# Optimization experiments

Hardware: AMD Instinct MI355X
Metric: run time of the kernel (lower is better)

The kernel has to match this reference:

```python
import jax, jax.numpy as jnp
import numpy as np
import math

B, S, D_EMB = 1, 4096, 768
N_HEADS, D_QKV = 12, 64
INV_TEMP = 1.0


def setup_inputs() -> dict:
    key = jax.random.key(0)
    ks = jax.random.split(key, 11)
    s = 0.02
    return {
        "q_in": jax.random.normal(ks[0], (B, S, D_EMB), jnp.float32),
        "k_in": jax.random.normal(ks[1], (B, S, D_EMB), jnp.float32),
        "v_in": jax.random.normal(ks[2], (B, S, D_EMB), jnp.float32),
        "W_q": jax.random.normal(ks[3], (D_EMB, N_HEADS * D_QKV), jnp.float32) * s,
        "b_q": jnp.zeros((N_HEADS * D_QKV,), jnp.float32),
        "W_k": jax.random.normal(ks[4], (D_EMB, N_HEADS * D_QKV), jnp.float32) * s,
        "b_k": jnp.zeros((N_HEADS * D_QKV,), jnp.float32),
        "W_v": jax.random.normal(ks[5], (D_EMB, N_HEADS * D_QKV), jnp.float32) * s,
        "b_v": jnp.zeros((N_HEADS * D_QKV,), jnp.float32),
        "W_o": jax.random.normal(ks[6], (N_HEADS * D_QKV, D_EMB), jnp.float32) * s,
        "b_o": jnp.zeros((D_EMB,), jnp.float32),
    }


def _split_heads(x):  # [B,S,H*D] -> [B,H,S,D]
    b, s, _ = x.shape
    return x.reshape(b, s, N_HEADS, D_QKV).transpose(0, 2, 1, 3)


def reference(q_in, k_in, v_in, W_q, b_q, W_k, b_k, W_v, b_v, W_o, b_o):
    q = _split_heads(q_in @ W_q + b_q)
    k = _split_heads(k_in @ W_k + b_k)
    v = _split_heads(v_in @ W_v + b_v)
    # full [B,H,S,S] score matrix (module materializes it for custom masking)
    scores = INV_TEMP * jnp.einsum('bhqd,bhkd->bhqk', q, k) / math.sqrt(D_QKV)
    attn = jax.nn.softmax(scores, axis=-1)
    out = jnp.einsum('bhqk,bhkd->bhqd', attn, v)  # [B,H,S,D]
    out = out.transpose(0, 2, 1, 3).reshape(q_in.shape[0], q_in.shape[1], N_HEADS * D_QKV)
    return out @ W_o + b_o
```

## Files before the change

### kernel.cpp

```cpp
#include <hip/hip_runtime.h>

#define S 4096
#define E 768
#define NH 12
#define DH 64
#define QSCALE (0.125f * 1.44269504f)
#define KSPLIT 4

typedef __bf16 bf16;
typedef __bf16 bf16x4 __attribute__((ext_vector_type(4)));
typedef __bf16 bf16x8 __attribute__((ext_vector_type(8)));
typedef float  f32x4  __attribute__((ext_vector_type(4)));

#define MFMA(a, b, c) __builtin_amdgcn_mfma_f32_16x16x32_bf16(a, b, c, 0, 0, 0)

__device__ __forceinline__ void async16(const bf16* g, bf16* l) {
  __builtin_amdgcn_global_load_lds(
      (const __attribute__((address_space(1))) void*)g,
      (__attribute__((address_space(3))) void*)l, 16, 0, 0);
}

__global__ __launch_bounds__(256) void prologue(const float* __restrict__ q_in,
                                                const float* __restrict__ k_in,
                                                const float* __restrict__ v_in,
                                                const float* __restrict__ w0,
                                                const float* __restrict__ w1,
                                                const float* __restrict__ w2,
                                                const float* __restrict__ w3,
                                                bf16* __restrict__ qb,
                                                bf16* __restrict__ kb,
                                                bf16* __restrict__ vb,
                                                bf16* __restrict__ t0,
                                                bf16* __restrict__ t1,
                                                bf16* __restrict__ t2,
                                                bf16* __restrict__ t3) {
  const int bid = blockIdx.x, tid = threadIdx.x;
  if (bid < 2304) {
    const int z = bid / 576, rem = bid % 576;
    const int bx = rem % 24, by = rem / 24;
    const float* W = z == 0 ? w0 : (z == 1 ? w1 : (z == 2 ? w2 : w3));
    bf16* Wt = z == 0 ? t0 : (z == 1 ? t1 : (z == 2 ? t2 : t3));
    __shared__ float t[32][33];
    const int tx = tid & 31, ty = tid >> 5;
    for (int j = ty; j < 32; j += 8)
      t[j][tx] = W[(by * 32 + j) * E + bx * 32 + tx];
    __syncthreads();
    for (int j = ty; j < 32; j += 8)
      Wt[(bx * 32 + j) * E + by * 32 + tx] = (bf16)t[tx][j];
  } else {
    const int b2 = bid - 2304;
    const int z = b2 / 3072, r2 = b2 % 3072;
    const float* in = z == 0 ? q_in : (z == 1 ? k_in : v_in);
    bf16* out = z == 0 ? qb : (z == 1 ? kb : vb);
    const int i = r2 * 1024 + tid * 4;
    float4 v = *(const float4*)(in + i);
    bf16x4 o = { (bf16)v.x, (bf16)v.y, (bf16)v.z, (bf16)v.w };
    *(bf16x4*)(out + i) = o;
  }
}

__global__ __launch_bounds__(256) void gemm128(const bf16* __restrict__ A0,
                                               const bf16* __restrict__ A1,
                                               const bf16* __restrict__ A2,
                                               const bf16* __restrict__ B0,
                                               const bf16* __restrict__ B1,
                                               const bf16* __restrict__ B2,
                                               const float* __restrict__ bias0,
                                               const float* __restrict__ bias1,
                                               const float* __restrict__ bias2,
                                               bf16* __restrict__ C0,
                                               bf16* __restrict__ C1,
                                               bf16* __restrict__ C2) {
  __shared__ __align__(16) bf16 smem[128 * 136];
  bf16* Asm = smem;
  bf16* Bsm = smem + 4096;
  bf16* Cs  = smem;

  const int z = blockIdx.z;
  const bf16* A  = z == 0 ? A0 : (z == 1 ? A1 : A2);
  const bf16* Bt = z == 0 ? B0 : (z == 1 ? B1 : B2);
  const float* bias = z == 0 ? bias0 : (z == 1 ? bias1 : bias2);

  const int tid = threadIdx.x;
  const int wv = tid >> 6, lane = tid & 63;
  const int quad = lane >> 4, l16 = lane & 15;
  const int m0 = blockIdx.x * 128, n0 = blockIdx.y * 128;
  const int wm = (wv >> 1) * 64, wn = (wv & 1) * 64;
  const int srow = lane >> 2, scol = (lane & 3) * 8;

  f32x4 acc[4][4] = {};

  for (int k0 = 0; k0 < E; k0 += 32) {
#pragma unroll
    for (int j = 0; j < 2; j++) {
      const int ch = wv * 2 + j;
      async16(&A[(size_t)(m0 + ch * 16 + srow) * E + k0 + scol], &Asm[ch * 512]);
      async16(&Bt[(size_t)(n0 + ch * 16 + srow) * E + k0 + scol], &Bsm[ch * 512]);
    }
    __syncthreads();
    bf16x8 af[4], bfv[4];
#pragma unroll
    for (int mi = 0; mi < 4; mi++)
      af[mi] = *(const bf16x8*)&Asm[(wm + mi * 16 + l16) * 32 + quad * 8];
#pragma unroll
    for (int ni = 0; ni < 4; ni++)
      bfv[ni] = *(const bf16x8*)&Bsm[(wn + ni * 16 + l16) * 32 + quad * 8];
#pragma unroll
    for (int mi = 0; mi < 4; mi++)
#pragma unroll
      for (int ni = 0; ni < 4; ni++)
        acc[mi][ni] = MFMA(af[mi], bfv[ni], acc[mi][ni]);
    __syncthreads();
  }

  const float scale = (z == 0) ? QSCALE : 1.0f;
#pragma unroll
  for (int mi = 0; mi < 4; mi++) {
#pragma unroll
    for (int ni = 0; ni < 4; ni++) {
      const int nl = wn + ni * 16 + l16;
      const float bv = bias[n0 + nl];
#pragma unroll
      for (int r = 0; r < 4; r++) {
        const int ml = wm + mi * 16 + quad * 4 + r;
        const float v = (acc[mi][ni][r] + bv) * scale;
        if (z == 2) Cs[nl * 136 + ml] = (bf16)v;
        else        Cs[ml * 136 + nl] = (bf16)v;
      }
    }
  }
  __syncthreads();

  if (z == 0) {
    const int e = lane & 7;
#pragma unroll
    for (int p = 0; p < 8; p++) {
      const int hr = p * 32 + wv * 8 + (lane >> 3);
      const int r = hr >> 1, hf = hr & 1;
      bf16x8 c = *(const bf16x8*)&Cs[r * 136 + hf * 64 + e * 8];
      *(bf16x8*)(C0 + (size_t)((n0 >> 6) + hf) * S * DH + (size_t)(m0 + r) * DH + e * 8) = c;
    }
  } else {
    bf16* dst = (z == 1) ? C1 : C2;
#pragma unroll
    for (int p = 0; p < 8; p++) {
      const int cid = p * 4 + wv;
      const int reg = cid >> 3;
      const int i = cid & 7;
      const int h_l = reg >> 1, tile = reg & 1;
      bf16x8 c;
      if (z == 1) {
        const int row = tile * 64 + (i >> 1) * 16 + l16;
        const int col = h_l * 64 + (i & 1) * 32 + quad * 8;
        c = *(const bf16x8*)&Cs[row * 136 + col];
      } else {
        const int nl = h_l * 64 + (i >> 1) * 16 + l16;
        const int ml = tile * 64 + (i & 1) * 32 + quad * 8;
        c = *(const bf16x8*)&Cs[nl * 136 + ml];
      }
      *(bf16x8*)(dst + (size_t)((n0 >> 6) + h_l) * S * DH +
                 (size_t)((m0 >> 6) + tile) * 4096 + i * 512 + lane * 8) = c;
    }
  }
}

__global__ __launch_bounds__(256, 3) void attn(const bf16* __restrict__ Q,
                                               const bf16* __restrict__ Kf,
                                               const bf16* __restrict__ Vf,
                                               bf16* __restrict__ Op0,
                                               bf16* __restrict__ Op1,
                                               bf16* __restrict__ Op2,
                                               bf16* __restrict__ Op3,
                                               float* __restrict__ Lp) {
  __shared__ __align__(16) bf16 P2[4][64][72];
  const int h = blockIdx.y, ks = blockIdx.z;
  const int tid = threadIdx.x;
  const int wave = tid >> 6, lane = tid & 63;
  const int quad = lane >> 4, l16 = lane & 15;
  const int q0 = blockIdx.x * 256 + wave * 64;

  const bf16* Qh = Q + (size_t)h * S * DH;
  const bf16* kbase = Kf + (size_t)h * S * DH + (size_t)ks * (S / KSPLIT) * DH + lane * 8;
  const bf16* vbase = Vf + (size_t)h * S * DH + (size_t)ks * (S / KSPLIT) * DH + lane * 8;
  bf16* Op = ks == 0 ? Op0 : (ks == 1 ? Op1 : (ks == 2 ? Op2 : Op3));

  bf16x8 aq[4][2];
#pragma unroll
  for (int qb = 0; qb < 4; qb++)
#pragma unroll
    for (int j = 0; j < 2; j++)
      aq[qb][j] = *(const bf16x8*)&Qh[(size_t)(q0 + qb * 16 + l16) * DH + j * 32 + quad * 8];

  bf16x8 ones;
#pragma unroll
  for (int e = 0; e < 8; e++) ones[e] = (bf16)1.0f;

  f32x4 o[4][4] = {};
  f32x4 ol[4] = {};

  bf16* Pw = &P2[wave][0][0];

  const int T = (S / KSPLIT) / 64;
  for (int t = 0; t < T; ++t) {
    const bf16* kp = kbase + (size_t)t * 4096;
    bf16x8 kr[8];
#pragma unroll
    for (int i = 0; i < 8; i++) kr[i] = *(const bf16x8*)(kp + i * 512);

#pragma unroll
    for (int kb = 0; kb < 4; kb++)
#pragma unroll
      for (int qb = 0; qb < 4; qb++) {
        f32x4 st = {};
        st = MFMA(kr[kb * 2], aq[qb][0], st);
        st = MFMA(kr[kb * 2 + 1], aq[qb][1], st);
        bf16x4 pk;
#pragma unroll
        for (int r = 0; r < 4; r++) pk[r] = (bf16)__builtin_exp2f(st[r]);
        *(bf16x4*)&Pw[(qb * 16 + l16) * 72 + kb * 16 + quad * 4] = pk;
      }

    bf16x8 bp[4][2];
#pragma unroll
    for (int qb = 0; qb < 4; qb++)
#pragma unroll
      for (int jc = 0; jc < 2; jc++)
        bp[qb][jc] = *(const bf16x8*)&Pw[(qb * 16 + l16) * 72 + jc * 32 + quad * 8];

#pragma unroll
    for (int qb = 0; qb < 4; qb++) {
      ol[qb] = MFMA(ones, bp[qb][0], ol[qb]);
      ol[qb] = MFMA(ones, bp[qb][1], ol[qb]);
    }

    const bf16* vp = vbase + (size_t)t * 4096;
#pragma unroll
    for (int db = 0; db < 4; db++) {
      bf16x8 v0 = *(const bf16x8*)(vp + (db * 2) * 512);
      bf16x8 v1 = *(const bf16x8*)(vp + (db * 2 + 1) * 512);
#pragma unroll
      for (int qb = 0; qb < 4; qb++) {
        o[db][qb] = MFMA(v0, bp[qb][0], o[db][qb]);
        o[db][qb] = MFMA(v1, bp[qb][1], o[db][qb]);
      }
    }
  }

  float* Lph = Lp + (size_t)(ks * NH + h) * S;
  if (quad == 0) {
#pragma unroll
    for (int qb = 0; qb < 4; qb++)
      Lph[q0 + qb * 16 + l16] = ol[qb][0];
  }
#pragma unroll
  for (int db = 0; db < 4; db++)
#pragma unroll
    for (int qb = 0; qb < 4; qb++) {
      bf16x4 pk;
#pragma unroll
      for (int r = 0; r < 4; r++) pk[r] = (bf16)o[db][qb][r];
      *(bf16x4*)&Pw[(qb * 16 + l16) * 72 + db * 16 + quad * 4] = pk;
    }
  {
    const int rr = lane >> 3, ee = (lane & 7) * 8;
#pragma unroll
    for (int p = 0; p < 8; p++) {
      const int row = p * 8 + rr;
      bf16x8 c = *(const bf16x8*)&Pw[row * 72 + ee];
      *(bf16x8*)(Op + (size_t)(q0 + row) * E + h * DH + ee) = c;
    }
  }
}

__global__ __launch_bounds__(256) void combine(const bf16* __restrict__ Op0,
                                               const bf16* __restrict__ Op1,
                                               const bf16* __restrict__ Op2,
                                               const bf16* __restrict__ Op3,
                                               const float* __restrict__ Lp,
                                               bf16* __restrict__ Obf) {
  const int i8 = blockIdx.x * 256 + threadIdx.x;
  const size_t base = (size_t)i8 * 8;
  const int row = (int)(base / E), c = (int)(base % E);
  const int h = c >> 6;
  const float l = Lp[(size_t)h * S + row] + Lp[(size_t)(NH + h) * S + row] +
                  Lp[(size_t)(2 * NH + h) * S + row] + Lp[(size_t)(3 * NH + h) * S + row];
  const float rl = 1.0f / l;
  bf16x8 a = *(const bf16x8*)(Op0 + base);
  bf16x8 b = *(const bf16x8*)(Op1 + base);
  bf16x8 cc = *(const bf16x8*)(Op2 + base);
  bf16x8 d = *(const bf16x8*)(Op3 + base);
  bf16x8 o;
#pragma unroll
  for (int e = 0; e < 8; e++)
    o[e] = (bf16)((((float)a[e] + (float)b[e]) + ((float)cc[e] + (float)d[e])) * rl);
  *(bf16x8*)(Obf + base) = o;
}

__global__ __launch_bounds__(256) void gemm64(const bf16* __restrict__ A,
                                              const bf16* __restrict__ Bt,
                                              const float* __restrict__ bias,
                                              float* __restrict__ C) {
  __shared__ __align__(16) bf16 Asm[2][64 * 32];
  __shared__ __align__(16) bf16 Bsm[2][64 * 32];
  const int tid = threadIdx.x;
  const int wv = tid >> 6, lane = tid & 63;
  const int quad = lane >> 4, l16 = lane & 15;
  const int m0 = blockIdx.x * 64, n0 = blockIdx.y * 64;
  const int srow = lane >> 2, scol = (lane & 3) * 8;

  f32x4 acc[4] = {};

  for (int k0 = 0; k0 < E; k0 += 64) {
#pragma unroll
    for (int jc = 0; jc < 2; jc++) {
      async16(&A[(size_t)(m0 + wv * 16 + srow) * E + k0 + jc * 32 + scol], &Asm[jc][wv * 512]);
      async16(&Bt[(size_t)(n0 + wv * 16 + srow) * E + k0 + jc * 32 + scol], &Bsm[jc][wv * 512]);
    }
    __syncthreads();
#pragma unroll
    for (int jc = 0; jc < 2; jc++) {
      bf16x8 af = *(const bf16x8*)&Asm[jc][(wv * 16 + l16) * 32 + quad * 8];
#pragma unroll
      for (int ni = 0; ni < 4; ni++) {
        bf16x8 bfr = *(const bf16x8*)&Bsm[jc][(ni * 16 + l16) * 32 + quad * 8];
        acc[ni] = MFMA(af, bfr, acc[ni]);
      }
    }
    __syncthreads();
  }

  const int row0 = m0 + wv * 16 + quad * 4;
#pragma unroll
  for (int ni = 0; ni < 4; ni++) {
    const int col = n0 + ni * 16 + l16;
    const float bv = bias[col];
#pragma unroll
    for (int r = 0; r < 4; r++)
      C[(size_t)(row0 + r) * E + col] = acc[ni][r] + bv;
  }
}

extern "C" void kernel_launch(void* const* d_in, const int* in_sizes, int n_in,
                              void* d_out, int out_size, void* d_ws, size_t ws_size,
                              hipStream_t stream) {
  (void)in_sizes; (void)n_in; (void)out_size; (void)ws_size;
  const float* q_in = (const float*)d_in[0];
  const float* k_in = (const float*)d_in[1];
  const float* v_in = (const float*)d_in[2];
  const float* W_q  = (const float*)d_in[3];
  const float* b_q  = (const float*)d_in[4];
  const float* W_k  = (const float*)d_in[5];
  const float* b_k  = (const float*)d_in[6];
  const float* W_v  = (const float*)d_in[7];
  const float* b_v  = (const float*)d_in[8];
  const float* W_o  = (const float*)d_in[9];
  const float* b_o  = (const float*)d_in[10];

  const size_t SE2 = (size_t)S * E * 2;
  const size_t EE2 = (size_t)E * E * 2;
  char* ws = (char*)d_ws;
  bf16* qb  = (bf16*)(ws);
  bf16* kb  = (bf16*)(ws + SE2);
  bf16* vb  = (bf16*)(ws + 2 * SE2);
  bf16* WqT = (bf16*)(ws + 3 * SE2);
  bf16* WkT = (bf16*)(ws + 3 * SE2 + EE2);
  bf16* WvT = (bf16*)(ws + 3 * SE2 + 2 * EE2);
  bf16* WoT = (bf16*)(ws + 3 * SE2 + 3 * EE2);
  bf16* Qh  = (bf16*)(ws + 3 * SE2 + 4 * EE2);
  bf16* Kf  = (bf16*)(ws + 4 * SE2 + 4 * EE2);
  bf16* Vf  = (bf16*)(ws + 5 * SE2 + 4 * EE2);
  bf16* Obf = (bf16*)(ws + 6 * SE2 + 4 * EE2);
  bf16* Op1 = qb;
  bf16* Op2 = kb;
  bf16* Op3 = vb;
  float* Lp = (float*)WqT;

  prologue<<<dim3(2304 + 3 * 3072), 256, 0, stream>>>(
      q_in, k_in, v_in, W_q, W_k, W_v, W_o, qb, kb, vb, WqT, WkT, WvT, WoT);

  gemm128<<<dim3(S / 128, E / 128, 3), 256, 0, stream>>>(
      qb, kb, vb, WqT, WkT, WvT, b_q, b_k, b_v, Qh, Kf, Vf);

  attn<<<dim3(S / 256, NH, KSPLIT), 256, 0, stream>>>(Qh, Kf, Vf, Obf, Op1, Op2, Op3, Lp);

  combine<<<dim3(S * E / 2048), 256, 0, stream>>>(Obf, Op1, Op2, Op3, Lp, Obf);

  gemm64<<<dim3(S / 64, E / 64), 256, 0, stream>>>(Obf, WoT, b_o, (float*)d_out);
}
```

Before: 228.5 us.

## Double-buffer K/V tiles in LDS via async loads and swizzle block order

```diff
diff --git a/kernel.cpp b/kernel.cpp
--- a/kernel.cpp
+++ b/kernel.cpp
@@ -172,17 +172,37 @@
                                                bf16* __restrict__ Op2,
                                                bf16* __restrict__ Op3,
                                                float* __restrict__ Lp) {
-  __shared__ __align__(16) bf16 P2[4][64][72];
-  const int h = blockIdx.y, ks = blockIdx.z;
+  __shared__ __align__(16) bf16 Kbuf[2][4096];
+  __shared__ __align__(16) bf16 Vbuf[2][4096];
+  __shared__ __align__(16) bf16 P2[4][32][72];
+
+  const int flat = blockIdx.x + 16 * (blockIdx.y + 12 * blockIdx.z);
+  const int swz = (flat & 7) * 96 + (flat >> 3);
+  const int qt = swz & 15;
+  const int rem = swz >> 4;
+  const int ks = rem & 3;
+  const int h = rem >> 2;
+
   const int tid = threadIdx.x;
   const int wave = tid >> 6, lane = tid & 63;
   const int quad = lane >> 4, l16 = lane & 15;
-  const int q0 = blockIdx.x * 256 + wave * 64;
+  const int q0 = qt * 256 + wave * 64;
 
   const bf16* Qh = Q + (size_t)h * S * DH;
-  const bf16* kbase = Kf + (size_t)h * S * DH + (size_t)ks * (S / KSPLIT) * DH + lane * 8;
-  const bf16* vbase = Vf + (size_t)h * S * DH + (size_t)ks * (S / KSPLIT) * DH + lane * 8;
+  const bf16* kbase = Kf + (size_t)h * S * DH + (size_t)ks * (S / KSPLIT) * DH;
+  const bf16* vbase = Vf + (size_t)h * S * DH + (size_t)ks * (S / KSPLIT) * DH;
   bf16* Op = ks == 0 ? Op0 : (ks == 1 ? Op1 : (ks == 2 ? Op2 : Op3));
+
+  auto stageKV = [&](int buf, int t) {
+    const bf16* kg = kbase + (size_t)t * 4096 + wave * 1024 + lane * 8;
+    const bf16* vg = vbase + (size_t)t * 4096 + wave * 1024 + lane * 8;
+    async16(kg,       &Kbuf[buf][wave * 1024]);
+    async16(kg + 512, &Kbuf[buf][wave * 1024 + 512]);
+    async16(vg,       &Vbuf[buf][wave * 1024]);
+    async16(vg + 512, &Vbuf[buf][wave * 1024 + 512]);
+  };
+
+  stageKV(0, 0);
 
   bf16x8 aq[4][2];
 #pragma unroll
@@ -202,48 +222,62 @@
 
   const int T = (S / KSPLIT) / 64;
   for (int t = 0; t < T; ++t) {
-    const bf16* kp = kbase + (size_t)t * 4096;
+    if (t + 1 < T) {
+      stageKV((t + 1) & 1, t + 1);
+      asm volatile("s_waitcnt vmcnt(4)" ::: "memory");
+    } else {
+      asm volatile("s_waitcnt vmcnt(0)" ::: "memory");
+    }
+    asm volatile("s_barrier" ::: "memory");
+
+    const bf16* kp = &Kbuf[t & 1][lane * 8];
+    const bf16* vp = &Vbuf[t & 1][lane * 8];
     bf16x8 kr[8];
 #pragma unroll
     for (int i = 0; i < 8; i++) kr[i] = *(const bf16x8*)(kp + i * 512);
 
 #pragma unroll
-    for (int kb = 0; kb < 4; kb++)
-#pragma unroll
-      for (int qb = 0; qb < 4; qb++) {
-        f32x4 st = {};
-        st = MFMA(kr[kb * 2], aq[qb][0], st);
-        st = MFMA(kr[kb * 2 + 1], aq[qb][1], st);
-        bf16x4 pk;
-#pragma unroll
-        for (int r = 0; r < 4; r++) pk[r] = (bf16)__builtin_exp2f(st[r]);
-        *(bf16x4*)&Pw[(qb * 16 + l16) * 72 + kb * 16 + quad * 4] = pk;
-      }
-
-    bf16x8 bp[4][2];
-#pragma unroll
-    for (int qb = 0; qb < 4; qb++)
-#pragma unroll
-      for (int jc = 0; jc < 2; jc++)
-        bp[qb][jc] = *(const bf16x8*)&Pw[(qb * 16 + l16) * 72 + jc * 32 + quad * 8];
-
-#pragma unroll
-    for (int qb = 0; qb < 4; qb++) {
-      ol[qb] = MFMA(ones, bp[qb][0], ol[qb]);
-      ol[qb] = MFMA(ones, bp[qb][1], ol[qb]);
-    }
-
-    const bf16* vp = vbase + (size_t)t * 4096;
-#pragma unroll
-    for (int db = 0; db < 4; db++) {
-      bf16x8 v0 = *(const bf16x8*)(vp + (db * 2) * 512);
-      bf16x8 v1 = *(const bf16x8*)(vp + (db * 2 + 1) * 512);
-#pragma unroll
-      for (int qb = 0; qb < 4; qb++) {
-        o[db][qb] = MFMA(v0, bp[qb][0], o[db][qb]);
-        o[db][qb] = MFMA(v1, bp[qb][1], o[db][qb]);
-      }
-    }
+    for (int half = 0; half < 2; half++) {
+#pragma unroll
+      for (int kb = 0; kb < 4; kb++)
+#pragma unroll
+        for (int q2 = 0; q2 < 2; q2++) {
+          const int qb = half * 2 + q2;
+          f32x4 st = {};
+          st = MFMA(kr[kb * 2], aq[qb][0], st);
+          st = MFMA(kr[kb * 2 + 1], aq[qb][1], st);
+          bf16x4 pk;
+#pragma unroll
+          for (int r = 0; r < 4; r++) pk[r] = (bf16)__builtin_exp2f(st[r]);
+          *(bf16x4*)&Pw[(q2 * 16 + l16) * 72 + kb * 16 + quad * 4] = pk;
+        }
+
+      bf16x8 bp[2][2];
+#pragma unroll
+      for (int q2 = 0; q2 < 2; q2++)
+#pragma unroll
+        for (int jc = 0; jc < 2; jc++)
+          bp[q2][jc] = *(const bf16x8*)&Pw[(q2 * 16 + l16) * 72 + jc * 32 + quad * 8];
+
+#pragma unroll
+      for (int q2 = 0; q2 < 2; q2++) {
+        ol[half * 2 + q2] = MFMA(ones, bp[q2][0], ol[half * 2 + q2]);
+        ol[half * 2 + q2] = MFMA(ones, bp[q2][1], ol[half * 2 + q2]);
+      }
+
+#pragma unroll
+      for (int db = 0; db < 4; db++) {
+        bf16x8 v0 = *(const bf16x8*)(vp + (db * 2) * 512);
+        bf16x8 v1 = *(const bf16x8*)(vp + (db * 2 + 1) * 512);
+#pragma unroll
+        for (int q2 = 0; q2 < 2; q2++) {
+          o[db][half * 2 + q2] = MFMA(v0, bp[q2][0], o[db][half * 2 + q2]);
+          o[db][half * 2 + q2] = MFMA(v1, bp[q2][1], o[db][half * 2 + q2]);
+        }
+      }
+    }
+
+    asm volatile("s_barrier" ::: "memory");
   }
 
   float* Lph = Lp + (size_t)(ks * NH + h) * S;
@@ -253,21 +287,22 @@
       Lph[q0 + qb * 16 + l16] = ol[qb][0];
   }
 #pragma unroll
-  for (int db = 0; db < 4; db++)
-#pragma unroll
-    for (int qb = 0; qb < 4; qb++) {
-      bf16x4 pk;
-#pragma unroll
-      for (int r = 0; r < 4; r++) pk[r] = (bf16)o[db][qb][r];
-      *(bf16x4*)&Pw[(qb * 16 + l16) * 72 + db * 16 + quad * 4] = pk;
-    }
-  {
+  for (int half = 0; half < 2; half++) {
+#pragma unroll
+    for (int db = 0; db < 4; db++)
+#pragma unroll
+      for (int q2 = 0; q2 < 2; q2++) {
+        bf16x4 pk;
+#pragma unroll
+        for (int r = 0; r < 4; r++) pk[r] = (bf16)o[db][half * 2 + q2][r];
+        *(bf16x4*)&Pw[(q2 * 16 + l16) * 72 + db * 16 + quad * 4] = pk;
+      }
     const int rr = lane >> 3, ee = (lane & 7) * 8;
 #pragma unroll
-    for (int p = 0; p < 8; p++) {
+    for (int p = 0; p < 4; p++) {
       const int row = p * 8 + rr;
       bf16x8 c = *(const bf16x8*)&Pw[row * 72 + ee];
-      *(bf16x8*)(Op + (size_t)(q0 + row) * E + h * DH + ee) = c;
+      *(bf16x8*)(Op + (size_t)(q0 + half * 32 + row) * E + h * DH + ee) = c;
     }
   }
 }
```

Result: slower. 239.9 us (+5.0%).
